# Optimization experiments

Measured on AMD Instinct MI355X. Metric: run time of the kernel, lower is better.

Reference implementation:

```python
import jax, jax.numpy as jnp
import numpy as np

HIDDEN = 896
N_HEADS = 14
N_KV = 2
HEAD_DIM = HIDDEN // N_HEADS  # 64
N_REP = N_HEADS // N_KV       # 7
ROPE_THETA = 1000000.0


def setup_inputs() -> dict:
    key = jax.random.key(0)
    ks = jax.random.split(key, 8)
    B, S = 2, 2048
    s = 0.02
    return {
        "hidden_states": jax.random.normal(ks[0], (B, S, HIDDEN), dtype=jnp.float32),
        "position_ids": jnp.broadcast_to(jnp.arange(S, dtype=jnp.int64), (B, S)),
        "Wq": jax.random.normal(ks[1], (HIDDEN, HIDDEN), dtype=jnp.float32) * s,
        "bq": jnp.zeros((HIDDEN,), dtype=jnp.float32),
        "Wk": jax.random.normal(ks[2], (N_KV * HEAD_DIM, HIDDEN), dtype=jnp.float32) * s,
        "bk": jnp.zeros((N_KV * HEAD_DIM,), dtype=jnp.float32),
        "Wv": jax.random.normal(ks[3], (N_KV * HEAD_DIM, HIDDEN), dtype=jnp.float32) * s,
        "bv": jnp.zeros((N_KV * HEAD_DIM,), dtype=jnp.float32),
        "Wo": jax.random.normal(ks[4], (HIDDEN, HIDDEN), dtype=jnp.float32) * s,
    }


def _rotate_half(x):
    x1, x2 = x[..., : HEAD_DIM // 2], x[..., HEAD_DIM // 2 :]
    return jnp.concatenate((-x2, x1), axis=-1)


def reference(hidden_states, position_ids, Wq, bq, Wk, bk, Wv, bv, Wo):
    B, S, _ = hidden_states.shape
    q = (hidden_states @ Wq.T + bq).reshape(B, S, N_HEADS, HEAD_DIM)
    k = (hidden_states @ Wk.T + bk).reshape(B, S, N_KV, HEAD_DIM)
    v = (hidden_states @ Wv.T + bv).reshape(B, S, N_KV, HEAD_DIM)

    # RoPE: cos/sin [B, S, 1, HEAD_DIM]
    inv_freq = 1.0 / (ROPE_THETA ** (jnp.arange(0, HEAD_DIM, 2, dtype=jnp.float32) / HEAD_DIM))
    freqs = position_ids.astype(jnp.float32)[..., None] * inv_freq  # [B,S,D/2]
    emb = jnp.concatenate((freqs, freqs), axis=-1)
    cos = jnp.cos(emb)[:, :, None, :]
    sin = jnp.sin(emb)[:, :, None, :]
    q = q * cos + _rotate_half(q) * sin
    k = k * cos + _rotate_half(k) * sin

    # [B, H, S, D]; repeat KV heads (GQA)
    q = q.transpose(0, 2, 1, 3)
    k = jnp.repeat(k.transpose(0, 2, 1, 3), N_REP, axis=1)
    v = jnp.repeat(v.transpose(0, 2, 1, 3), N_REP, axis=1)

    scale = 1.0 / np.sqrt(HEAD_DIM)
    scores = jnp.einsum("bhqd,bhkd->bhqk", q, k) * scale
    causal = jnp.tril(jnp.ones((S, S), dtype=bool))
    scores = jnp.where(causal[None, None, :, :], scores, jnp.finfo(scores.dtype).min)
    probs = jax.nn.softmax(scores, axis=-1)
    attn = jnp.einsum("bhqk,bhkd->bhqd", probs, v)  # [B,H,S,D]
    attn = attn.transpose(0, 2, 1, 3).reshape(B, S, HIDDEN)
    return attn @ Wo.T
```

## Files before the change

### kernel.cpp

```cpp
#include <hip/hip_runtime.h>

#define HID 896
#define NH 14
#define NKV 2
#define NREP 7
#define SEQ 2048
#define BT 2
#define NTOK (BT*SEQ)
#define CSCALE 0.18033688011112042f

typedef __attribute__((ext_vector_type(8))) short bf16x8;
typedef __attribute__((ext_vector_type(8))) unsigned short u16x8;
typedef __attribute__((ext_vector_type(4))) float fx4;
typedef __attribute__((ext_vector_type(4))) short s16x4;
typedef _Float16 f16x4 __attribute__((ext_vector_type(4)));
typedef __fp16 fp16x2 __attribute__((ext_vector_type(2)));

__device__ __forceinline__ unsigned short f2b(float x){
  union { float f; unsigned u; } a; a.f = x;
  unsigned r = a.u + 0x7FFFu + ((a.u >> 16) & 1u);
  return (unsigned short)(r >> 16);
}
__device__ __forceinline__ unsigned short f2h(float x){
  union { _Float16 h; unsigned short u; } a; a.h = (_Float16)x; return a.u;
}

__device__ __forceinline__ void gll16(const unsigned short* g, short* lds){
  __builtin_amdgcn_global_load_lds(
      (const __attribute__((address_space(1))) unsigned int*)(const void*)g,
      (__attribute__((address_space(3))) unsigned int*)(void*)lds, 16, 0, 0);
}

__global__ __launch_bounds__(256) void cvt_kernel(
    const float* __restrict__ s0, const float* __restrict__ s1,
    const float* __restrict__ s2, const float* __restrict__ s3,
    const float* __restrict__ s4,
    unsigned short* __restrict__ d0, unsigned short* __restrict__ d1,
    unsigned short* __restrict__ d2, unsigned short* __restrict__ d3,
    unsigned short* __restrict__ d4,
    int c0, int c1, int c2, int c3, int c4,
    float2* __restrict__ tab)
{
  if (blockIdx.y == 5){
    for (int i = blockIdx.x*256 + threadIdx.x; i < SEQ*32; i += gridDim.x*256){
      int s = i >> 5, d = i & 31;
      float f = (float)s * exp2f(-(float)d * 0.62286151779138041f);
      float sv, cv; sincosf(f, &sv, &cv);
      tab[i] = make_float2(cv, sv);
    }
    return;
  }
  const float* s; unsigned short* d; int c;
  switch (blockIdx.y){
    case 0: s=s0; d=d0; c=c0; break;
    case 1: s=s1; d=d1; c=c1; break;
    case 2: s=s2; d=d2; c=c2; break;
    case 3: s=s3; d=d3; c=c3; break;
    default: s=s4; d=d4; c=c4; break;
  }
  for (int i = (blockIdx.x*256 + threadIdx.x)*8; i < c; i += gridDim.x*2048){
    float4 a = *(const float4*)(s + i);
    float4 b = *(const float4*)(s + i + 4);
    u16x8 o;
    o[0]=f2b(a.x); o[1]=f2b(a.y); o[2]=f2b(a.z); o[3]=f2b(a.w);
    o[4]=f2b(b.x); o[5]=f2b(b.y); o[6]=f2b(b.z); o[7]=f2b(b.w);
    *(u16x8*)(d + i) = o;
  }
}

__global__ __launch_bounds__(256) void qkv_gemm_kernel(
    const unsigned short* __restrict__ A, const unsigned short* __restrict__ Bw,
    const float* __restrict__ bq, const float* __restrict__ bk, const float* __restrict__ bv,
    const int* __restrict__ pos, const float2* __restrict__ tab,
    unsigned short* __restrict__ qo, unsigned short* __restrict__ ko,
    unsigned short* __restrict__ vt)
{
  __shared__ short As[2][64*64];
  __shared__ short Bs[2][128*64];
  const int tid = threadIdx.x;
  const int bm = blockIdx.x, bn = blockIdx.y;
  const int w = tid >> 6, l = tid & 63, l15 = l & 15, q4 = l >> 4;
  const int wm = w >> 1, wn = w & 1;
  const int lr = l >> 3;
  const int cbg = (l & 7) ^ lr;
  const int sw = l15 & 7;

  fx4 acc[2][4] = {};

  const unsigned short* Ag = A  + (size_t)(bm*64)*HID;
  const unsigned short* Bg = Bw + (size_t)(bn*128)*HID;

  auto issue = [&](int kt, int buf){
    const int kc = kt*64 + cbg*8;
#pragma unroll
    for (int p = 0; p < 2; p++){
      int c = p*4 + w;
      gll16(Ag + (size_t)(c*8 + lr)*HID + kc, &As[buf][c*512]);
    }
#pragma unroll
    for (int p = 0; p < 4; p++){
      int c = p*4 + w;
      gll16(Bg + (size_t)(c*8 + lr)*HID + kc, &Bs[buf][c*512]);
    }
  };

  issue(0, 0);
  for (int kt = 0; kt < 14; kt++){
    const int cur = kt & 1;
    if (kt < 13){
      issue(kt+1, cur^1);
      asm volatile("s_waitcnt vmcnt(6)\n\ts_barrier" ::: "memory");
    } else {
      asm volatile("s_waitcnt vmcnt(0)\n\ts_barrier" ::: "memory");
    }
#pragma unroll
    for (int ks = 0; ks < 2; ks++){
      bf16x8 af[2], bf[4];
#pragma unroll
      for (int mt = 0; mt < 2; mt++){
        int r = wm*32 + mt*16 + l15;
        af[mt] = *(bf16x8*)&As[cur][r*64 + ((ks*4 + q4) ^ sw)*8];
      }
#pragma unroll
      for (int nt = 0; nt < 4; nt++){
        int r = wn*64 + nt*16 + l15;
        bf[nt] = *(bf16x8*)&Bs[cur][r*64 + ((ks*4 + q4) ^ sw)*8];
      }
#pragma unroll
      for (int mt = 0; mt < 2; mt++)
#pragma unroll
        for (int nt = 0; nt < 4; nt++)
          acc[mt][nt] = __builtin_amdgcn_mfma_f32_16x16x32_bf16(af[mt], bf[nt], acc[mt][nt], 0,0,0);
    }
    asm volatile("s_barrier" ::: "memory");
  }

  const int hu = bn*2 + wn;
  const float* bias; int kind, hloc;
  if (hu < NH)      { bias = bq + hu*64;      kind = 0; hloc = hu; }
  else if (hu < 16) { bias = bk + (hu-NH)*64; kind = 1; hloc = hu-NH; }
  else              { bias = bv + (hu-16)*64; kind = 2; hloc = hu-16; }
  float bl[4];
#pragma unroll
  for (int nt = 0; nt < 4; nt++) bl[nt] = bias[nt*16 + l15];

  if (kind == 2){
#pragma unroll
    for (int mt = 0; mt < 2; mt++)
#pragma unroll
      for (int j = 0; j < 4; j++){
        int grow = bm*64 + wm*32 + mt*16 + q4*4 + j;
        int b = grow >> 11, s = grow & (SEQ-1);
        int tile = s >> 6, key = s & 63;
        unsigned short* dst = vt + (size_t)(((b*NKV + hloc)*(SEQ/64) + tile)*4096);
#pragma unroll
        for (int nt = 0; nt < 4; nt++)
          dst[(nt*16 + l15)*64 + key] = f2h(acc[mt][nt][j] + bl[nt]);
      }
  } else {
    const float qs = (kind == 0) ? CSCALE : 1.0f;
#pragma unroll
    for (int mt = 0; mt < 2; mt++)
#pragma unroll
      for (int j = 0; j < 4; j++){
        int grow = bm*64 + wm*32 + mt*16 + q4*4 + j;
        int b = grow >> 11, s = grow & (SEQ-1);
        int p = pos[grow];
        const float2* rp = tab + p*32 + l15;
        float2 cs0 = rp[0], cs1 = rp[16];
        unsigned short* dst = (kind == 0)
            ? qo + ((size_t)(b*NH  + hloc)*SEQ + s)*64
            : ko + ((size_t)(b*NKV + hloc)*SEQ + s)*64;
        float x1 = acc[mt][0][j] + bl[0], x2 = acc[mt][2][j] + bl[2];
        float y1 = acc[mt][1][j] + bl[1], y2 = acc[mt][3][j] + bl[3];
        dst[l15]      = f2b((x1*cs0.x - x2*cs0.y)*qs);
        dst[16 + l15] = f2b((y1*cs1.x - y2*cs1.y)*qs);
        dst[32 + l15] = f2b((x2*cs0.x + x1*cs0.y)*qs);
        dst[48 + l15] = f2b((y2*cs1.x + y1*cs1.y)*qs);
      }
  }
}

__device__ __forceinline__ void smax_pv(
    const fx4* s, bool diag, int wl, int q4,
    float& m_run, float& l_run, fx4* o, const f16x4 vf[4][4])
{
  float tv[16];
#pragma unroll
  for (int tl = 0; tl < 4; tl++)
#pragma unroll
    for (int j = 0; j < 4; j++){
      float x = s[tl][j];
      if (diag && (tl*16 + q4*4 + j > wl)) x = -1e30f;
      tv[tl*4+j] = x;
    }
  float mx = tv[0];
#pragma unroll
  for (int i = 1; i < 16; i++) mx = fmaxf(mx, tv[i]);
  mx = fmaxf(mx, __shfl_xor(mx, 16));
  mx = fmaxf(mx, __shfl_xor(mx, 32));
  float mn = fmaxf(m_run, mx);
  float al = exp2f(m_run - mn);
  m_run = mn;
  float p[16], rs = 0.f;
#pragma unroll
  for (int i = 0; i < 16; i++){ p[i] = exp2f(tv[i] - mn); rs += p[i]; }
  rs += __shfl_xor(rs, 16);
  rs += __shfl_xor(rs, 32);
  l_run = l_run*al + rs;
#pragma unroll
  for (int nt = 0; nt < 4; nt++)
#pragma unroll
    for (int j = 0; j < 4; j++) o[nt][j] *= al;
  f16x4 pf[4];
#pragma unroll
  for (int tl = 0; tl < 4; tl++){
    union { f16x4 v; fp16x2 h[2]; } u;
    u.h[0] = __builtin_amdgcn_cvt_pkrtz(p[tl*4+0], p[tl*4+1]);
    u.h[1] = __builtin_amdgcn_cvt_pkrtz(p[tl*4+2], p[tl*4+3]);
    pf[tl] = u.v;
  }
#pragma unroll
  for (int nt = 0; nt < 4; nt++)
#pragma unroll
    for (int tl = 0; tl < 4; tl++)
      o[nt] = __builtin_amdgcn_mfma_f32_16x16x16f16(vf[nt][tl], pf[tl], o[nt], 0,0,0);
}

__global__ __launch_bounds__(512) void attn_kernel(
    const unsigned short* __restrict__ q, const unsigned short* __restrict__ k,
    const unsigned short* __restrict__ vt, unsigned short* __restrict__ ao)
{
  __shared__ short SB[4*64*72];
  short* KsB = SB;
  short* VtB = SB + 2*64*72;

  const int tid = threadIdx.x;
  const int w = tid >> 6, l = tid & 63, l15 = l & 15, q4 = l >> 4;
  const int g = w >> 2, wi = w & 3;
  const int tlo = blockIdx.x, thi = 31 - tlo;
  const int h = blockIdx.y, b = blockIdx.z, kvh = h / NREP;
  const int wl = wi*16 + l15;

  const unsigned short* qbase = q + ((size_t)(b*NH + h)*SEQ)*64;
  const unsigned short* qpA = qbase + (size_t)(thi*64 + wl)*64;
  const unsigned short* qpB = qbase + (size_t)(tlo*64 + wl)*64;
  bf16x8 qA0 = *(const bf16x8*)(qpA + q4*8), qA1 = *(const bf16x8*)(qpA + 32 + q4*8);
  bf16x8 qB0 = *(const bf16x8*)(qpB + q4*8), qB1 = *(const bf16x8*)(qpB + 32 + q4*8);

  fx4 oA[4] = {}, oB[4] = {};
  float mA = -1e30f, lA = 0.f, mB = -1e30f, lB = 0.f;

  const unsigned short* kbase = k  + ((size_t)(b*NKV + kvh)*SEQ)*64;
  const unsigned short* vbase = vt + (size_t)((b*NKV + kvh)*(SEQ/64))*4096;

  const int P = (thi + 2) >> 1;

  u16x8 kreg[2], vreg[2];
#pragma unroll
  for (int p = 0; p < 2; p++){
    int idx = p*512 + tid, tile = idx >> 9, off = idx & 511;
    kreg[p] = *(const u16x8*)(kbase + (size_t)tile*4096 + off*8);
    vreg[p] = *(const u16x8*)(vbase + (size_t)tile*4096 + off*8);
  }

  for (int si = 0; si < P; si++){
#pragma unroll
    for (int p = 0; p < 2; p++){
      int idx = p*512 + tid, tile = idx >> 9, off = idx & 511;
      int rr = off >> 3, g8 = off & 7;
      *(u16x8*)&KsB[tile*4608 + rr*72 + g8*8] = kreg[p];
      *(u16x8*)&VtB[tile*4608 + rr*72 + g8*8] = vreg[p];
    }
    __syncthreads();

    if (si + 1 < P){
      const int k0n = 2*(si+1);
#pragma unroll
      for (int p = 0; p < 2; p++){
        int idx = p*512 + tid, tile = idx >> 9, off = idx & 511;
        int tk = k0n + tile; if (tk > thi) tk = thi;
        kreg[p] = *(const u16x8*)(kbase + (size_t)tk*4096 + off*8);
        vreg[p] = *(const u16x8*)(vbase + (size_t)tk*4096 + off*8);
      }
    }

    const int kt = 2*si + g;
    if (kt <= thi){
      const short* Kst = KsB + g*4608;
      const short* Vtt = VtB + g*4608;
      bf16x8 kf0[4], kf1[4];
#pragma unroll
      for (int tl = 0; tl < 4; tl++){
        kf0[tl] = *(const bf16x8*)&Kst[(tl*16 + l15)*72 + q4*8];
        kf1[tl] = *(const bf16x8*)&Kst[(tl*16 + l15)*72 + 32 + q4*8];
      }
      f16x4 vf[4][4];
#pragma unroll
      for (int nt = 0; nt < 4; nt++)
#pragma unroll
        for (int tl = 0; tl < 4; tl++)
          vf[nt][tl] = *(const f16x4*)&Vtt[(nt*16 + l15)*72 + tl*16 + q4*4];

      {
        fx4 s[4] = {};
#pragma unroll
        for (int tl = 0; tl < 4; tl++){
          s[tl] = __builtin_amdgcn_mfma_f32_16x16x32_bf16(kf0[tl], qA0, s[tl], 0,0,0);
          s[tl] = __builtin_amdgcn_mfma_f32_16x16x32_bf16(kf1[tl], qA1, s[tl], 0,0,0);
        }
        smax_pv(s, kt == thi, wl, q4, mA, lA, oA, vf);
      }
      if (kt <= tlo){
        fx4 s[4] = {};
#pragma unroll
        for (int tl = 0; tl < 4; tl++){
          s[tl] = __builtin_amdgcn_mfma_f32_16x16x32_bf16(kf0[tl], qB0, s[tl], 0,0,0);
          s[tl] = __builtin_amdgcn_mfma_f32_16x16x32_bf16(kf1[tl], qB1, s[tl], 0,0,0);
        }
        smax_pv(s, kt == tlo, wl, q4, mB, lB, oB, vf);
      }
    }
    __syncthreads();
  }

  float* F = (float*)SB;
  if (g == 1){
    float* fa = F + (((wi*2 + 0)*64 + l)*18);
#pragma unroll
    for (int nt = 0; nt < 4; nt++)
#pragma unroll
      for (int j = 0; j < 4; j++) fa[nt*4 + j] = oA[nt][j];
    fa[16] = mA; fa[17] = lA;
    float* fb = F + (((wi*2 + 1)*64 + l)*18);
#pragma unroll
    for (int nt = 0; nt < 4; nt++)
#pragma unroll
      for (int j = 0; j < 4; j++) fb[nt*4 + j] = oB[nt][j];
    fb[16] = mB; fb[17] = lB;
  }
  __syncthreads();
  if (g == 0){
    {
      const float* fa = F + (((wi*2 + 0)*64 + l)*18);
      float m1 = fa[16], l1 = fa[17];
      float mM = fmaxf(mA, m1);
      float a0 = exp2f(mA - mM), a1 = exp2f(m1 - mM);
      lA = lA*a0 + l1*a1;
#pragma unroll
      for (int nt = 0; nt < 4; nt++)
#pragma unroll
        for (int j = 0; j < 4; j++) oA[nt][j] = oA[nt][j]*a0 + fa[nt*4+j]*a1;
    }
    {
      const float* fb = F + (((wi*2 + 1)*64 + l)*18);
      float m1 = fb[16], l1 = fb[17];
      float mM = fmaxf(mB, m1);
      float a0 = exp2f(mB - mM), a1 = exp2f(m1 - mM);
      lB = lB*a0 + l1*a1;
#pragma unroll
      for (int nt = 0; nt < 4; nt++)
#pragma unroll
        for (int j = 0; j < 4; j++) oB[nt][j] = oB[nt][j]*a0 + fb[nt*4+j]*a1;
    }
    {
      float inv = 1.0f / lA;
      unsigned short* dst = ao + ((size_t)(b*SEQ + thi*64 + wl))*HID + h*64;
#pragma unroll
      for (int nt = 0; nt < 4; nt++){
        s16x4 ov;
        ov[0] = (short)f2b(oA[nt][0]*inv); ov[1] = (short)f2b(oA[nt][1]*inv);
        ov[2] = (short)f2b(oA[nt][2]*inv); ov[3] = (short)f2b(oA[nt][3]*inv);
        *(s16x4*)(dst + nt*16 + q4*4) = ov;
      }
    }
    {
      float inv = 1.0f / lB;
      unsigned short* dst = ao + ((size_t)(b*SEQ + tlo*64 + wl))*HID + h*64;
#pragma unroll
      for (int nt = 0; nt < 4; nt++){
        s16x4 ov;
        ov[0] = (short)f2b(oB[nt][0]*inv); ov[1] = (short)f2b(oB[nt][1]*inv);
        ov[2] = (short)f2b(oB[nt][2]*inv); ov[3] = (short)f2b(oB[nt][3]*inv);
        *(s16x4*)(dst + nt*16 + q4*4) = ov;
      }
    }
  }
}

__global__ __launch_bounds__(256) void out_gemm_kernel(
    const unsigned short* __restrict__ A, const unsigned short* __restrict__ Bw,
    float* __restrict__ out)
{
  __shared__ short As[2][64*64];
  __shared__ short Bs[2][128*64];
  const int tid = threadIdx.x;
  const int bm = blockIdx.x, bn = blockIdx.y;
  const int w = tid >> 6, l = tid & 63, l15 = l & 15, q4 = l >> 4;
  const int wm = w >> 1, wn = w & 1;
  const int lr = l >> 3;
  const int cbg = (l & 7) ^ lr;
  const int sw = l15 & 7;

  fx4 acc[2][4] = {};

  const unsigned short* Ag = A  + (size_t)(bm*64)*HID;
  const unsigned short* Bg = Bw + (size_t)(bn*128)*HID;

  auto issue = [&](int kt, int buf){
    const int kc = kt*64 + cbg*8;
#pragma unroll
    for (int p = 0; p < 2; p++){
      int c = p*4 + w;
      gll16(Ag + (size_t)(c*8 + lr)*HID + kc, &As[buf][c*512]);
    }
#pragma unroll
    for (int p = 0; p < 4; p++){
      int c = p*4 + w;
      gll16(Bg + (size_t)(c*8 + lr)*HID + kc, &Bs[buf][c*512]);
    }
  };

  issue(0, 0);
  for (int kt = 0; kt < 14; kt++){
    const int cur = kt & 1;
    if (kt < 13){
      issue(kt+1, cur^1);
      asm volatile("s_waitcnt vmcnt(6)\n\ts_barrier" ::: "memory");
    } else {
      asm volatile("s_waitcnt vmcnt(0)\n\ts_barrier" ::: "memory");
    }
#pragma unroll
    for (int ks = 0; ks < 2; ks++){
      bf16x8 af[2], bf[4];
#pragma unroll
      for (int mt = 0; mt < 2; mt++){
        int r = wm*32 + mt*16 + l15;
        af[mt] = *(bf16x8*)&As[cur][r*64 + ((ks*4 + q4) ^ sw)*8];
      }
#pragma unroll
      for (int nt = 0; nt < 4; nt++){
        int r = wn*64 + nt*16 + l15;
        bf[nt] = *(bf16x8*)&Bs[cur][r*64 + ((ks*4 + q4) ^ sw)*8];
      }
#pragma unroll
      for (int mt = 0; mt < 2; mt++)
#pragma unroll
        for (int nt = 0; nt < 4; nt++)
          acc[mt][nt] = __builtin_amdgcn_mfma_f32_16x16x32_bf16(af[mt], bf[nt], acc[mt][nt], 0,0,0);
    }
    asm volatile("s_barrier" ::: "memory");
  }

#pragma unroll
  for (int mt = 0; mt < 2; mt++)
#pragma unroll
    for (int j = 0; j < 4; j++){
      int grow = bm*64 + wm*32 + mt*16 + q4*4 + j;
      float* dst = out + (size_t)grow*HID + bn*128 + wn*64;
#pragma unroll
      for (int nt = 0; nt < 4; nt++)
        dst[nt*16 + l15] = acc[mt][nt][j];
    }
}

extern "C" void kernel_launch(void* const* d_in, const int* in_sizes, int n_in,
                              void* d_out, int out_size, void* d_ws, size_t ws_size,
                              hipStream_t stream)
{
  const float* hidden = (const float*)d_in[0];
  const int*   pos    = (const int*)d_in[1];
  const float* Wq = (const float*)d_in[2]; const float* bq = (const float*)d_in[3];
  const float* Wk = (const float*)d_in[4]; const float* bk = (const float*)d_in[5];
  const float* Wv = (const float*)d_in[6]; const float* bv = (const float*)d_in[7];
  const float* Wo = (const float*)d_in[8];

  unsigned short* qws   = (unsigned short*)d_ws;
  unsigned short* kws   = qws   + (size_t)BT*NH*SEQ*64;
  unsigned short* vtws  = kws   + (size_t)BT*NKV*SEQ*64;
  unsigned short* wqkv  = vtws  + (size_t)BT*NKV*SEQ*64;
  unsigned short* wo16  = wqkv  + (size_t)1152*HID;
  unsigned short* h16   = wo16  + (size_t)HID*HID;
  float2*         tab   = (float2*)(h16 + (size_t)NTOK*HID);

  const int nh   = NTOK*HID;
  const int nwq  = HID*HID;
  const int nwkv = 2*64*HID;

  cvt_kernel<<<dim3(448, 6), 256, 0, stream>>>(
      hidden, Wq, Wk, Wv, Wo,
      h16, wqkv, wqkv + nwq, wqkv + nwq + nwkv, wo16,
      nh, nwq, nwkv, nwkv, nwq, tab);

  qkv_gemm_kernel<<<dim3(NTOK/64, 9), 256, 0, stream>>>(
      h16, wqkv, bq, bk, bv, pos, tab, qws, kws, vtws);

  attn_kernel<<<dim3(16, NH, BT), 512, 0, stream>>>(qws, kws, vtws, h16);

  out_gemm_kernel<<<dim3(NTOK/64, 7), 256, 0, stream>>>(h16, wo16, (float*)d_out);
}
```

Before: 163.8 us.

## Load K/V fragments directly from global memory instead of staging through LDS

Drops the shared-memory staging of K and V tiles, together with the register prefetch and per-iteration barriers. Each wave group now reads its MFMA fragments straight from global memory (relying on L1/L2 for reuse across the four waves sharing a tile). The softmax and PV steps are also split so both query tiles' softmax runs before the PV MFMAs, which allows more interleaving. The risk is many small, uncoalesced global loads with exposed latency and no explicit prefetch, in exchange for removing the LDS traffic and syncs.

```diff
diff --git a/kernel.cpp b/kernel.cpp
--- a/kernel.cpp
+++ b/kernel.cpp
@@ -181,9 +181,9 @@
   }
 }
 
-__device__ __forceinline__ void smax_pv(
+__device__ __forceinline__ void smax_part(
     const fx4* s, bool diag, int wl, int q4,
-    float& m_run, float& l_run, fx4* o, const f16x4 vf[4][4])
+    float& m_run, float& l_run, fx4* o, f16x4* pf)
 {
   float tv[16];
 #pragma unroll
@@ -212,7 +212,6 @@
   for (int nt = 0; nt < 4; nt++)
 #pragma unroll
     for (int j = 0; j < 4; j++) o[nt][j] *= al;
-  f16x4 pf[4];
 #pragma unroll
   for (int tl = 0; tl < 4; tl++){
     union { f16x4 v; fp16x2 h[2]; } u;
@@ -220,6 +219,10 @@
     u.h[1] = __builtin_amdgcn_cvt_pkrtz(p[tl*4+2], p[tl*4+3]);
     pf[tl] = u.v;
   }
+}
+
+__device__ __forceinline__ void pv_part(fx4* o, const f16x4 pf[4], const f16x4 vf[4][4])
+{
 #pragma unroll
   for (int nt = 0; nt < 4; nt++)
 #pragma unroll
@@ -231,9 +234,7 @@
     const unsigned short* __restrict__ q, const unsigned short* __restrict__ k,
     const unsigned short* __restrict__ vt, unsigned short* __restrict__ ao)
 {
-  __shared__ short SB[4*64*72];
-  short* KsB = SB;
-  short* VtB = SB + 2*64*72;
+  __shared__ float F[8*64*18];
 
   const int tid = threadIdx.x;
   const int w = tid >> 6, l = tid & 63, l15 = l & 15, q4 = l >> 4;
@@ -254,77 +255,46 @@
   const unsigned short* kbase = k  + ((size_t)(b*NKV + kvh)*SEQ)*64;
   const unsigned short* vbase = vt + (size_t)((b*NKV + kvh)*(SEQ/64))*4096;
 
-  const int P = (thi + 2) >> 1;
-
-  u16x8 kreg[2], vreg[2];
-#pragma unroll
-  for (int p = 0; p < 2; p++){
-    int idx = p*512 + tid, tile = idx >> 9, off = idx & 511;
-    kreg[p] = *(const u16x8*)(kbase + (size_t)tile*4096 + off*8);
-    vreg[p] = *(const u16x8*)(vbase + (size_t)tile*4096 + off*8);
-  }
-
-  for (int si = 0; si < P; si++){
-#pragma unroll
-    for (int p = 0; p < 2; p++){
-      int idx = p*512 + tid, tile = idx >> 9, off = idx & 511;
-      int rr = off >> 3, g8 = off & 7;
-      *(u16x8*)&KsB[tile*4608 + rr*72 + g8*8] = kreg[p];
-      *(u16x8*)&VtB[tile*4608 + rr*72 + g8*8] = vreg[p];
-    }
-    __syncthreads();
-
-    if (si + 1 < P){
-      const int k0n = 2*(si+1);
-#pragma unroll
-      for (int p = 0; p < 2; p++){
-        int idx = p*512 + tid, tile = idx >> 9, off = idx & 511;
-        int tk = k0n + tile; if (tk > thi) tk = thi;
-        kreg[p] = *(const u16x8*)(kbase + (size_t)tk*4096 + off*8);
-        vreg[p] = *(const u16x8*)(vbase + (size_t)tk*4096 + off*8);
-      }
-    }
-
-    const int kt = 2*si + g;
-    if (kt <= thi){
-      const short* Kst = KsB + g*4608;
-      const short* Vtt = VtB + g*4608;
-      bf16x8 kf0[4], kf1[4];
+  for (int kt = g; kt <= thi; kt += 2){
+    const unsigned short* kp = kbase + (size_t)kt*4096;
+    bf16x8 kf0[4], kf1[4];
+#pragma unroll
+    for (int tl = 0; tl < 4; tl++){
+      kf0[tl] = *(const bf16x8*)(kp + (tl*16 + l15)*64 + q4*8);
+      kf1[tl] = *(const bf16x8*)(kp + (tl*16 + l15)*64 + 32 + q4*8);
+    }
+    fx4 sA[4] = {};
+#pragma unroll
+    for (int tl = 0; tl < 4; tl++){
+      sA[tl] = __builtin_amdgcn_mfma_f32_16x16x32_bf16(kf0[tl], qA0, sA[tl], 0,0,0);
+      sA[tl] = __builtin_amdgcn_mfma_f32_16x16x32_bf16(kf1[tl], qA1, sA[tl], 0,0,0);
+    }
+    const bool doB = (kt <= tlo);
+    fx4 sB[4] = {};
+    if (doB){
 #pragma unroll
       for (int tl = 0; tl < 4; tl++){
-        kf0[tl] = *(const bf16x8*)&Kst[(tl*16 + l15)*72 + q4*8];
-        kf1[tl] = *(const bf16x8*)&Kst[(tl*16 + l15)*72 + 32 + q4*8];
-      }
-      f16x4 vf[4][4];
-#pragma unroll
-      for (int nt = 0; nt < 4; nt++)
-#pragma unroll
-        for (int tl = 0; tl < 4; tl++)
-          vf[nt][tl] = *(const f16x4*)&Vtt[(nt*16 + l15)*72 + tl*16 + q4*4];
-
-      {
-        fx4 s[4] = {};
-#pragma unroll
-        for (int tl = 0; tl < 4; tl++){
-          s[tl] = __builtin_amdgcn_mfma_f32_16x16x32_bf16(kf0[tl], qA0, s[tl], 0,0,0);
-          s[tl] = __builtin_amdgcn_mfma_f32_16x16x32_bf16(kf1[tl], qA1, s[tl], 0,0,0);
-        }
-        smax_pv(s, kt == thi, wl, q4, mA, lA, oA, vf);
-      }
-      if (kt <= tlo){
-        fx4 s[4] = {};
-#pragma unroll
-        for (int tl = 0; tl < 4; tl++){
-          s[tl] = __builtin_amdgcn_mfma_f32_16x16x32_bf16(kf0[tl], qB0, s[tl], 0,0,0);
-          s[tl] = __builtin_amdgcn_mfma_f32_16x16x32_bf16(kf1[tl], qB1, s[tl], 0,0,0);
-        }
-        smax_pv(s, kt == tlo, wl, q4, mB, lB, oB, vf);
-      }
-    }
-    __syncthreads();
-  }
-
-  float* F = (float*)SB;
+        sB[tl] = __builtin_amdgcn_mfma_f32_16x16x32_bf16(kf0[tl], qB0, sB[tl], 0,0,0);
+        sB[tl] = __builtin_amdgcn_mfma_f32_16x16x32_bf16(kf1[tl], qB1, sB[tl], 0,0,0);
+      }
+    }
+
+    const unsigned short* vp = vbase + (size_t)kt*4096;
+    f16x4 vf[4][4];
+#pragma unroll
+    for (int nt = 0; nt < 4; nt++)
+#pragma unroll
+      for (int tl = 0; tl < 4; tl++)
+        vf[nt][tl] = *(const f16x4*)(vp + (nt*16 + l15)*64 + tl*16 + q4*4);
+
+    f16x4 pfA[4], pfB[4];
+    smax_part(sA, kt == thi, wl, q4, mA, lA, oA, pfA);
+    if (doB) smax_part(sB, kt == tlo, wl, q4, mB, lB, oB, pfB);
+
+    pv_part(oA, pfA, vf);
+    if (doB) pv_part(oB, pfB, vf);
+  }
+
   if (g == 1){
     float* fa = F + (((wi*2 + 0)*64 + l)*18);
 #pragma unroll
```

New measurement: 285.2 us. +74.1%, slower.

## Fuse hidden-state bf16 conversion into QKV GEMM A-tile loading

Applied to the files above, without the earlier changes.

The separate fp32-to-bf16 conversion pass over the hidden states is removed. The QKV GEMM now reads fp32 activations directly into registers, converts them to bf16 and stores them into the swizzled LDS tile. The weight tile keeps its async global-to-LDS path. This removes a full write and re-read of the bf16 hidden copy, but the A tile no longer streams asynchronously into LDS, and the fp32 A data is re-read by each of the nine N-column blocks, doubling the bytes per read.

```diff
diff --git a/kernel.cpp b/kernel.cpp
--- a/kernel.cpp
+++ b/kernel.cpp
@@ -34,14 +34,12 @@
 __global__ __launch_bounds__(256) void cvt_kernel(
     const float* __restrict__ s0, const float* __restrict__ s1,
     const float* __restrict__ s2, const float* __restrict__ s3,
-    const float* __restrict__ s4,
     unsigned short* __restrict__ d0, unsigned short* __restrict__ d1,
     unsigned short* __restrict__ d2, unsigned short* __restrict__ d3,
-    unsigned short* __restrict__ d4,
-    int c0, int c1, int c2, int c3, int c4,
+    int c0, int c1, int c2, int c3,
     float2* __restrict__ tab)
 {
-  if (blockIdx.y == 5){
+  if (blockIdx.y == 4){
     for (int i = blockIdx.x*256 + threadIdx.x; i < SEQ*32; i += gridDim.x*256){
       int s = i >> 5, d = i & 31;
       float f = (float)s * exp2f(-(float)d * 0.62286151779138041f);
@@ -55,8 +53,7 @@
     case 0: s=s0; d=d0; c=c0; break;
     case 1: s=s1; d=d1; c=c1; break;
     case 2: s=s2; d=d2; c=c2; break;
-    case 3: s=s3; d=d3; c=c3; break;
-    default: s=s4; d=d4; c=c4; break;
+    default: s=s3; d=d3; c=c3; break;
   }
   for (int i = (blockIdx.x*256 + threadIdx.x)*8; i < c; i += gridDim.x*2048){
     float4 a = *(const float4*)(s + i);
@@ -69,7 +66,7 @@
 }
 
 __global__ __launch_bounds__(256) void qkv_gemm_kernel(
-    const unsigned short* __restrict__ A, const unsigned short* __restrict__ Bw,
+    const float* __restrict__ Ahid, const unsigned short* __restrict__ Bw,
     const float* __restrict__ bq, const float* __restrict__ bk, const float* __restrict__ bv,
     const int* __restrict__ pos, const float2* __restrict__ tab,
     unsigned short* __restrict__ qo, unsigned short* __restrict__ ko,
@@ -87,16 +84,33 @@
 
   fx4 acc[2][4] = {};
 
-  const unsigned short* Ag = A  + (size_t)(bm*64)*HID;
-  const unsigned short* Bg = Bw + (size_t)(bn*128)*HID;
-
-  auto issue = [&](int kt, int buf){
+  const float*          Ag = Ahid + (size_t)(bm*64)*HID;
+  const unsigned short* Bg = Bw   + (size_t)(bn*128)*HID;
+
+  float4 Areg[2][2];
+  auto loadA = [&](int kt){
     const int kc = kt*64 + cbg*8;
+#pragma unroll
+    for (int p = 0; p < 2; p++){
+      const float* src = Ag + (size_t)((p*4 + w)*8 + lr)*HID + kc;
+      Areg[p][0] = *(const float4*)(src);
+      Areg[p][1] = *(const float4*)(src + 4);
+    }
+  };
+  auto storeA = [&](int buf){
 #pragma unroll
     for (int p = 0; p < 2; p++){
       int c = p*4 + w;
-      gll16(Ag + (size_t)(c*8 + lr)*HID + kc, &As[buf][c*512]);
-    }
+      u16x8 o;
+      o[0]=f2b(Areg[p][0].x); o[1]=f2b(Areg[p][0].y);
+      o[2]=f2b(Areg[p][0].z); o[3]=f2b(Areg[p][0].w);
+      o[4]=f2b(Areg[p][1].x); o[5]=f2b(Areg[p][1].y);
+      o[6]=f2b(Areg[p][1].z); o[7]=f2b(Areg[p][1].w);
+      *(u16x8*)&As[buf][c*512 + l*8] = o;
+    }
+  };
+  auto issueB = [&](int kt, int buf){
+    const int kc = kt*64 + cbg*8;
 #pragma unroll
     for (int p = 0; p < 4; p++){
       int c = p*4 + w;
@@ -104,15 +118,16 @@
     }
   };
 
-  issue(0, 0);
+  issueB(0, 0);
+  loadA(0);
   for (int kt = 0; kt < 14; kt++){
     const int cur = kt & 1;
+    storeA(cur);
     if (kt < 13){
-      issue(kt+1, cur^1);
-      asm volatile("s_waitcnt vmcnt(6)\n\ts_barrier" ::: "memory");
-    } else {
-      asm volatile("s_waitcnt vmcnt(0)\n\ts_barrier" ::: "memory");
-    }
+      issueB(kt+1, cur^1);
+      loadA(kt+1);
+    }
+    asm volatile("s_waitcnt lgkmcnt(0)\n\ts_barrier" ::: "memory");
 #pragma unroll
     for (int ks = 0; ks < 2; ks++){
       bf16x8 af[2], bf[4];
@@ -483,17 +498,16 @@
   unsigned short* h16   = wo16  + (size_t)HID*HID;
   float2*         tab   = (float2*)(h16 + (size_t)NTOK*HID);
 
-  const int nh   = NTOK*HID;
   const int nwq  = HID*HID;
   const int nwkv = 2*64*HID;
 
-  cvt_kernel<<<dim3(448, 6), 256, 0, stream>>>(
-      hidden, Wq, Wk, Wv, Wo,
-      h16, wqkv, wqkv + nwq, wqkv + nwq + nwkv, wo16,
-      nh, nwq, nwkv, nwkv, nwq, tab);
+  cvt_kernel<<<dim3(448, 5), 256, 0, stream>>>(
+      Wq, Wk, Wv, Wo,
+      wqkv, wqkv + nwq, wqkv + nwq + nwkv, wo16,
+      nwq, nwkv, nwkv, nwq, tab);
 
   qkv_gemm_kernel<<<dim3(NTOK/64, 9), 256, 0, stream>>>(
-      h16, wqkv, bq, bk, bv, pos, tab, qws, kws, vtws);
+      hidden, wqkv, bq, bk, bv, pos, tab, qws, kws, vtws);
 
   attn_kernel<<<dim3(16, NH, BT), 512, 0, stream>>>(qws, kws, vtws, h16);
 
```

New measurement: 167.5 us, median of 2. +2.3%, slower.

## Double-buffer K/V LDS tiles in attention and enlarge GEMM M-tiles to 128

Applied to the files above, without the earlier changes.

The attention kernel now keeps two LDS buffers for K/V tiles. The next tile's registers are written to the alternate buffer after compute, so each iteration needs one barrier instead of two. Both projection GEMMs move from 64-row to 128-row block tiles with a 4x4 accumulator per wave, which halves the grid and improves weight reuse. The costs are more LDS and registers per block, lower occupancy, and fewer blocks (256 for QKV, 224 for output) to spread across the CUs.

```diff
diff --git a/kernel.cpp b/kernel.cpp
--- a/kernel.cpp
+++ b/kernel.cpp
@@ -75,7 +75,7 @@
     unsigned short* __restrict__ qo, unsigned short* __restrict__ ko,
     unsigned short* __restrict__ vt)
 {
-  __shared__ short As[2][64*64];
+  __shared__ short As[2][128*64];
   __shared__ short Bs[2][128*64];
   const int tid = threadIdx.x;
   const int bm = blockIdx.x, bn = blockIdx.y;
@@ -85,15 +85,15 @@
   const int cbg = (l & 7) ^ lr;
   const int sw = l15 & 7;
 
-  fx4 acc[2][4] = {};
-
-  const unsigned short* Ag = A  + (size_t)(bm*64)*HID;
+  fx4 acc[4][4] = {};
+
+  const unsigned short* Ag = A  + (size_t)(bm*128)*HID;
   const unsigned short* Bg = Bw + (size_t)(bn*128)*HID;
 
   auto issue = [&](int kt, int buf){
     const int kc = kt*64 + cbg*8;
 #pragma unroll
-    for (int p = 0; p < 2; p++){
+    for (int p = 0; p < 4; p++){
       int c = p*4 + w;
       gll16(Ag + (size_t)(c*8 + lr)*HID + kc, &As[buf][c*512]);
     }
@@ -109,16 +109,16 @@
     const int cur = kt & 1;
     if (kt < 13){
       issue(kt+1, cur^1);
-      asm volatile("s_waitcnt vmcnt(6)\n\ts_barrier" ::: "memory");
+      asm volatile("s_waitcnt vmcnt(8)\n\ts_barrier" ::: "memory");
     } else {
       asm volatile("s_waitcnt vmcnt(0)\n\ts_barrier" ::: "memory");
     }
 #pragma unroll
     for (int ks = 0; ks < 2; ks++){
-      bf16x8 af[2], bf[4];
-#pragma unroll
-      for (int mt = 0; mt < 2; mt++){
-        int r = wm*32 + mt*16 + l15;
+      bf16x8 af[4], bf[4];
+#pragma unroll
+      for (int mt = 0; mt < 4; mt++){
+        int r = wm*64 + mt*16 + l15;
         af[mt] = *(bf16x8*)&As[cur][r*64 + ((ks*4 + q4) ^ sw)*8];
       }
 #pragma unroll
@@ -127,7 +127,7 @@
         bf[nt] = *(bf16x8*)&Bs[cur][r*64 + ((ks*4 + q4) ^ sw)*8];
       }
 #pragma unroll
-      for (int mt = 0; mt < 2; mt++)
+      for (int mt = 0; mt < 4; mt++)
 #pragma unroll
         for (int nt = 0; nt < 4; nt++)
           acc[mt][nt] = __builtin_amdgcn_mfma_f32_16x16x32_bf16(af[mt], bf[nt], acc[mt][nt], 0,0,0);
@@ -146,10 +146,10 @@
 
   if (kind == 2){
 #pragma unroll
-    for (int mt = 0; mt < 2; mt++)
+    for (int mt = 0; mt < 4; mt++)
 #pragma unroll
       for (int j = 0; j < 4; j++){
-        int grow = bm*64 + wm*32 + mt*16 + q4*4 + j;
+        int grow = bm*128 + wm*64 + mt*16 + q4*4 + j;
         int b = grow >> 11, s = grow & (SEQ-1);
         int tile = s >> 6, key = s & 63;
         unsigned short* dst = vt + (size_t)(((b*NKV + hloc)*(SEQ/64) + tile)*4096);
@@ -160,10 +160,10 @@
   } else {
     const float qs = (kind == 0) ? CSCALE : 1.0f;
 #pragma unroll
-    for (int mt = 0; mt < 2; mt++)
+    for (int mt = 0; mt < 4; mt++)
 #pragma unroll
       for (int j = 0; j < 4; j++){
-        int grow = bm*64 + wm*32 + mt*16 + q4*4 + j;
+        int grow = bm*128 + wm*64 + mt*16 + q4*4 + j;
         int b = grow >> 11, s = grow & (SEQ-1);
         int p = pos[grow];
         const float2* rp = tab + p*32 + l15;
@@ -231,9 +231,7 @@
     const unsigned short* __restrict__ q, const unsigned short* __restrict__ k,
     const unsigned short* __restrict__ vt, unsigned short* __restrict__ ao)
 {
-  __shared__ short SB[4*64*72];
-  short* KsB = SB;
-  short* VtB = SB + 2*64*72;
+  __shared__ short SB[8*64*72];
 
   const int tid = threadIdx.x;
   const int w = tid >> 6, l = tid & 63, l15 = l & 15, q4 = l >> 4;
@@ -258,37 +256,39 @@
 
   u16x8 kreg[2], vreg[2];
 #pragma unroll
-  for (int p = 0; p < 2; p++){
-    int idx = p*512 + tid, tile = idx >> 9, off = idx & 511;
-    kreg[p] = *(const u16x8*)(kbase + (size_t)tile*4096 + off*8);
-    vreg[p] = *(const u16x8*)(vbase + (size_t)tile*4096 + off*8);
+  for (int p2 = 0; p2 < 2; p2++){
+    int idx = p2*512 + tid, tile = idx >> 9, off = idx & 511;
+    kreg[p2] = *(const u16x8*)(kbase + (size_t)tile*4096 + off*8);
+    vreg[p2] = *(const u16x8*)(vbase + (size_t)tile*4096 + off*8);
+  }
+#pragma unroll
+  for (int p2 = 0; p2 < 2; p2++){
+    int idx = p2*512 + tid, tile = idx >> 9, off = idx & 511;
+    int rr = off >> 3, g8 = off & 7;
+    *(u16x8*)&SB[tile*4608 + rr*72 + g8*8] = kreg[p2];
+    *(u16x8*)&SB[9216 + tile*4608 + rr*72 + g8*8] = vreg[p2];
   }
 
   for (int si = 0; si < P; si++){
-#pragma unroll
-    for (int p = 0; p < 2; p++){
-      int idx = p*512 + tid, tile = idx >> 9, off = idx & 511;
-      int rr = off >> 3, g8 = off & 7;
-      *(u16x8*)&KsB[tile*4608 + rr*72 + g8*8] = kreg[p];
-      *(u16x8*)&VtB[tile*4608 + rr*72 + g8*8] = vreg[p];
-    }
-    __syncthreads();
-
-    if (si + 1 < P){
+    asm volatile("s_waitcnt lgkmcnt(0)\n\ts_barrier" ::: "memory");
+    const int p = si & 1;
+    const bool more = (si + 1 < P);
+
+    if (more){
       const int k0n = 2*(si+1);
 #pragma unroll
-      for (int p = 0; p < 2; p++){
-        int idx = p*512 + tid, tile = idx >> 9, off = idx & 511;
+      for (int p2 = 0; p2 < 2; p2++){
+        int idx = p2*512 + tid, tile = idx >> 9, off = idx & 511;
         int tk = k0n + tile; if (tk > thi) tk = thi;
-        kreg[p] = *(const u16x8*)(kbase + (size_t)tk*4096 + off*8);
-        vreg[p] = *(const u16x8*)(vbase + (size_t)tk*4096 + off*8);
+        kreg[p2] = *(const u16x8*)(kbase + (size_t)tk*4096 + off*8);
+        vreg[p2] = *(const u16x8*)(vbase + (size_t)tk*4096 + off*8);
       }
     }
 
     const int kt = 2*si + g;
     if (kt <= thi){
-      const short* Kst = KsB + g*4608;
-      const short* Vtt = VtB + g*4608;
+      const short* Kst = SB + p*18432 + g*4608;
+      const short* Vtt = SB + p*18432 + 9216 + g*4608;
       bf16x8 kf0[4], kf1[4];
 #pragma unroll
       for (int tl = 0; tl < 4; tl++){
@@ -321,8 +321,19 @@
         smax_pv(s, kt == tlo, wl, q4, mB, lB, oB, vf);
       }
     }
-    __syncthreads();
-  }
+
+    if (more){
+      const int pn = (si & 1) ^ 1;
+#pragma unroll
+      for (int p2 = 0; p2 < 2; p2++){
+        int idx = p2*512 + tid, tile = idx >> 9, off = idx & 511;
+        int rr = off >> 3, g8 = off & 7;
+        *(u16x8*)&SB[pn*18432 + tile*4608 + rr*72 + g8*8] = kreg[p2];
+        *(u16x8*)&SB[pn*18432 + 9216 + tile*4608 + rr*72 + g8*8] = vreg[p2];
+      }
+    }
+  }
+  __syncthreads();
 
   float* F = (float*)SB;
   if (g == 1){
@@ -392,7 +403,7 @@
     const unsigned short* __restrict__ A, const unsigned short* __restrict__ Bw,
     float* __restrict__ out)
 {
-  __shared__ short As[2][64*64];
+  __shared__ short As[2][128*64];
   __shared__ short Bs[2][128*64];
   const int tid = threadIdx.x;
   const int bm = blockIdx.x, bn = blockIdx.y;
@@ -402,15 +413,15 @@
   const int cbg = (l & 7) ^ lr;
   const int sw = l15 & 7;
 
-  fx4 acc[2][4] = {};
-
-  const unsigned short* Ag = A  + (size_t)(bm*64)*HID;
+  fx4 acc[4][4] = {};
+
+  const unsigned short* Ag = A  + (size_t)(bm*128)*HID;
   const unsigned short* Bg = Bw + (size_t)(bn*128)*HID;
 
   auto issue = [&](int kt, int buf){
     const int kc = kt*64 + cbg*8;
 #pragma unroll
-    for (int p = 0; p < 2; p++){
+    for (int p = 0; p < 4; p++){
       int c = p*4 + w;
       gll16(Ag + (size_t)(c*8 + lr)*HID + kc, &As[buf][c*512]);
     }
@@ -426,16 +437,16 @@
     const int cur = kt & 1;
     if (kt < 13){
       issue(kt+1, cur^1);
-      asm volatile("s_waitcnt vmcnt(6)\n\ts_barrier" ::: "memory");
+      asm volatile("s_waitcnt vmcnt(8)\n\ts_barrier" ::: "memory");
     } else {
       asm volatile("s_waitcnt vmcnt(0)\n\ts_barrier" ::: "memory");
     }
 #pragma unroll
     for (int ks = 0; ks < 2; ks++){
-      bf16x8 af[2], bf[4];
-#pragma unroll
-      for (int mt = 0; mt < 2; mt++){
-        int r = wm*32 + mt*16 + l15;
+      bf16x8 af[4], bf[4];
+#pragma unroll
+      for (int mt = 0; mt < 4; mt++){
+        int r = wm*64 + mt*16 + l15;
         af[mt] = *(bf16x8*)&As[cur][r*64 + ((ks*4 + q4) ^ sw)*8];
       }
 #pragma unroll
@@ -444,7 +455,7 @@
         bf[nt] = *(bf16x8*)&Bs[cur][r*64 + ((ks*4 + q4) ^ sw)*8];
       }
 #pragma unroll
-      for (int mt = 0; mt < 2; mt++)
+      for (int mt = 0; mt < 4; mt++)
 #pragma unroll
         for (int nt = 0; nt < 4; nt++)
           acc[mt][nt] = __builtin_amdgcn_mfma_f32_16x16x32_bf16(af[mt], bf[nt], acc[mt][nt], 0,0,0);
@@ -453,10 +464,10 @@
   }
 
 #pragma unroll
-  for (int mt = 0; mt < 2; mt++)
+  for (int mt = 0; mt < 4; mt++)
 #pragma unroll
     for (int j = 0; j < 4; j++){
-      int grow = bm*64 + wm*32 + mt*16 + q4*4 + j;
+      int grow = bm*128 + wm*64 + mt*16 + q4*4 + j;
       float* dst = out + (size_t)grow*HID + bn*128 + wn*64;
 #pragma unroll
       for (int nt = 0; nt < 4; nt++)
@@ -492,10 +503,10 @@
       h16, wqkv, wqkv + nwq, wqkv + nwq + nwkv, wo16,
       nh, nwq, nwkv, nwkv, nwq, tab);
 
-  qkv_gemm_kernel<<<dim3(NTOK/64, 9), 256, 0, stream>>>(
+  qkv_gemm_kernel<<<dim3(NTOK/128, 9), 256, 0, stream>>>(
       h16, wqkv, bq, bk, bv, pos, tab, qws, kws, vtws);
 
   attn_kernel<<<dim3(16, NH, BT), 512, 0, stream>>>(qws, kws, vtws, h16);
 
-  out_gemm_kernel<<<dim3(NTOK/64, 7), 256, 0, stream>>>(h16, wo16, (float*)d_out);
-}
+  out_gemm_kernel<<<dim3(NTOK/128, 7), 256, 0, stream>>>(h16, wo16, (float*)d_out);
+}
```

Result: slower. 174.7 us (+6.7%).
